# Kernel optimization log

Measured on AMD Instinct MI355X. Metric: run time of the kernel, lower is better.

## Reference

```python
import jax, jax.numpy as jnp
import numpy as np

B, L, D, U = 4, 1024, 64, 32

def setup_inputs() -> dict:
    key = jax.random.key(0)
    ks = jax.random.split(key, 6)
    inputs = jax.random.normal(ks[0], (B, L, D), dtype=jnp.float32)
    Wt = jax.random.normal(ks[1], (D, U), dtype=jnp.float32) * 0.1
    Wx = jax.random.normal(ks[2], (D, U), dtype=jnp.float32) * 0.1
    Wa = jax.random.normal(ks[3], (U, 1), dtype=jnp.float32) * 0.1
    bh = jax.random.normal(ks[4], (U,), dtype=jnp.float32) * 0.1
    ba = jax.random.normal(ks[5], (1,), dtype=jnp.float32) * 0.1
    return {"inputs": inputs, "Wt": Wt, "Wx": Wx, "Wa": Wa,
            "bh": bh, "ba": ba, "attention_width": 0}

def reference(inputs, Wt, Wx, Wa, bh, ba, attention_width):
    # Additive (Bahdanau) self-attention emission.
    q = inputs @ Wt                              # (B, L, U)
    k = inputs @ Wx                              # (B, L, U)
    # broadcast add -> (B, L, L, U), the dominant intermediate
    h = jnp.tanh(q[:, :, None, :] + k[:, None, :, :] + bh)
    e = jnp.squeeze(h @ Wa, axis=-1) + ba        # (B, L, L); ba broadcasts
    # NOTE: attention_width mask is dead code in the original forward -> ignored.
    # manual max-subtracted softmax with +1e-8 denominator (as in source)
    m = jnp.max(e, axis=-1, keepdims=True)
    ex = jnp.exp(e - m)
    a = ex / (jnp.sum(ex, axis=-1, keepdims=True) + 1e-8)
    v = jnp.einsum('bij,bjd->bid', a, inputs)    # (B, L, D)
    return v
```

## Files before the change

kernel.cpp:

```cpp
#include <hip/hip_runtime.h>

#define BB 4
#define LL 1024
#define DD 64
#define UU 32

__global__ __launch_bounds__(256) void precompute_kernel(
    const float* __restrict__ inp, const float* __restrict__ Wt,
    const float* __restrict__ Wx, const float* __restrict__ bh,
    float* __restrict__ Eq, float* __restrict__ Ek)
{
    __shared__ float s_in[8][DD];
    int t = threadIdx.x;
    int row0 = blockIdx.x * 8;
    if (t < 128) {
        ((float4*)s_in)[t] = ((const float4*)(inp + (size_t)row0 * DD))[t];
    }
    __syncthreads();
    int r = t >> 5;
    int u = t & 31;
    size_t row = row0 + r;
    float q = 0.f, k = 0.f;
#pragma unroll
    for (int d = 0; d < DD; ++d) {
        float x = s_in[r][d];
        q = fmaf(x, Wt[d * UU + u], q);
        k = fmaf(x, Wx[d * UU + u], k);
    }
    float eq = expf(2.f * (q + bh[u]));
    float ek = expf(2.f * k);
    Eq[row * UU + u] = eq;
    Ek[row * UU + u] = ek;
}

__device__ __forceinline__ float block_reduce_max(float v, float* sred, int t) {
#pragma unroll
    for (int m = 32; m >= 1; m >>= 1) v = fmaxf(v, __shfl_xor(v, m, 64));
    __syncthreads();
    if ((t & 63) == 0) sred[t >> 6] = v;
    __syncthreads();
    return fmaxf(fmaxf(sred[0], sred[1]), fmaxf(sred[2], sred[3]));
}
__device__ __forceinline__ float block_reduce_sum(float v, float* sred, int t) {
#pragma unroll
    for (int m = 32; m >= 1; m >>= 1) v += __shfl_xor(v, m, 64);
    __syncthreads();
    if ((t & 63) == 0) sred[t >> 6] = v;
    __syncthreads();
    return (sred[0] + sred[1]) + (sred[2] + sred[3]);
}

__global__ __launch_bounds__(256) void attn_kernel(
    const float* __restrict__ Eq, const float* __restrict__ Ek,
    const float* __restrict__ inp, const float* __restrict__ Wa,
    float* __restrict__ out)
{
    __shared__ float  s_a[LL][4];
    __shared__ float4 s_v[16][4][16];
    __shared__ float  s_red[4];

    int t  = threadIdx.x;
    int b  = blockIdx.x >> 8;
    int i0 = (blockIdx.x & 255) * 4;

    const float* ekb = Ek + (size_t)b * LL * UU;

    float e[4][4];
#pragma unroll
    for (int jj = 0; jj < 4; ++jj) {
        int j = jj * 256 + t;
        const float4* ekp = (const float4*)(ekb + (size_t)j * UU);
        float4 ekv[8];
#pragma unroll
        for (int u4 = 0; u4 < 8; ++u4) ekv[u4] = ekp[u4];
#pragma unroll
        for (int i = 0; i < 4; ++i) {
            const float* eqr = Eq + ((size_t)(b * LL + i0 + i)) * UU;
            float acc = 0.f;
#pragma unroll
            for (int u4 = 0; u4 < 8; ++u4) {
                const float* eqq = eqr + u4 * 4;
                const float* waq = Wa + u4 * 4;
                acc = fmaf(waq[0], __builtin_amdgcn_rcpf(fmaf(eqq[0], ekv[u4].x, 1.f)), acc);
                acc = fmaf(waq[1], __builtin_amdgcn_rcpf(fmaf(eqq[1], ekv[u4].y, 1.f)), acc);
                acc = fmaf(waq[2], __builtin_amdgcn_rcpf(fmaf(eqq[2], ekv[u4].z, 1.f)), acc);
                acc = fmaf(waq[3], __builtin_amdgcn_rcpf(fmaf(eqq[3], ekv[u4].w, 1.f)), acc);
            }
            e[i][jj] = -2.f * acc;
        }
    }

    float rs[4];
#pragma unroll
    for (int i = 0; i < 4; ++i) {
        float tm = fmaxf(fmaxf(e[i][0], e[i][1]), fmaxf(e[i][2], e[i][3]));
        float m = block_reduce_max(tm, s_red, t);
        float s = 0.f;
#pragma unroll
        for (int jj = 0; jj < 4; ++jj) {
            e[i][jj] = __expf(e[i][jj] - m);
            s += e[i][jj];
        }
        s = block_reduce_sum(s, s_red, t);
        rs[i] = 1.0f / (s + 1e-8f);
    }
#pragma unroll
    for (int jj = 0; jj < 4; ++jj) {
        float4 av;
        av.x = e[0][jj] * rs[0];
        av.y = e[1][jj] * rs[1];
        av.z = e[2][jj] * rs[2];
        av.w = e[3][jj] * rs[3];
        ((float4*)s_a)[jj * 256 + t] = av;
    }
    __syncthreads();

    int dq = t & 15;
    int g  = t >> 4;
    const float4* inp4 = (const float4*)(inp + (size_t)b * LL * DD);
    float4 v0 = {0,0,0,0}, v1 = {0,0,0,0}, v2 = {0,0,0,0}, v3 = {0,0,0,0};
#pragma unroll 4
    for (int jj = 0; jj < 64; ++jj) {
        int j = jj * 16 + g;
        float4 x  = inp4[j * 16 + dq];
        const float* ap = &s_a[j][0];
        float a0 = ap[0], a1 = ap[1], a2 = ap[2], a3 = ap[3];
        v0.x = fmaf(a0, x.x, v0.x); v0.y = fmaf(a0, x.y, v0.y);
        v0.z = fmaf(a0, x.z, v0.z); v0.w = fmaf(a0, x.w, v0.w);
        v1.x = fmaf(a1, x.x, v1.x); v1.y = fmaf(a1, x.y, v1.y);
        v1.z = fmaf(a1, x.z, v1.z); v1.w = fmaf(a1, x.w, v1.w);
        v2.x = fmaf(a2, x.x, v2.x); v2.y = fmaf(a2, x.y, v2.y);
        v2.z = fmaf(a2, x.z, v2.z); v2.w = fmaf(a2, x.w, v2.w);
        v3.x = fmaf(a3, x.x, v3.x); v3.y = fmaf(a3, x.y, v3.y);
        v3.z = fmaf(a3, x.z, v3.z); v3.w = fmaf(a3, x.w, v3.w);
    }
    s_v[g][0][dq] = v0;
    s_v[g][1][dq] = v1;
    s_v[g][2][dq] = v2;
    s_v[g][3][dq] = v3;
    __syncthreads();

    int i = t >> 6;
    int d = t & 63;
    const float* svf = (const float*)s_v;
    float r = 0.f;
#pragma unroll
    for (int g2 = 0; g2 < 16; ++g2) r += svf[g2 * 256 + i * 64 + d];
    out[((size_t)b * LL + (i0 + i)) * DD + d] = r;
}

extern "C" void kernel_launch(void* const* d_in, const int* in_sizes, int n_in,
                              void* d_out, int out_size, void* d_ws, size_t ws_size,
                              hipStream_t stream) {
    const float* inp = (const float*)d_in[0];
    const float* Wt  = (const float*)d_in[1];
    const float* Wx  = (const float*)d_in[2];
    const float* Wa  = (const float*)d_in[3];
    const float* bh  = (const float*)d_in[4];
    float* out = (float*)d_out;

    float* Eq = (float*)d_ws;
    float* Ek = Eq + (size_t)BB * LL * UU;

    precompute_kernel<<<BB * LL / 8, 256, 0, stream>>>(inp, Wt, Wx, bh, Eq, Ek);
    attn_kernel<<<BB * LL / 4, 256, 0, stream>>>(Eq, Ek, inp, Wa, out);
}
```

Baseline: 102.1 us.

## Combine four reciprocals into one, batch softmax reductions, stage weights in LDS

The attention score loop now merges four rcp(1+eq*ek) terms into one fraction, so a single reciprocal per four units replaces four. The Ek loads are reordered so each u4 chunk is prefetched across all four j columns. The per-row max and sum reductions are batched so each needs one pair of barriers instead of eight. The precompute kernel stages Wt and Wx in shared memory and uses fast exp. LDS for the probability and partial-output buffers is overlapped through a union, which adds an extra barrier. Multiplying four denominators together could overflow for large exponent values.

Measured after the change: 100.8 us. About the same (-1.2%).

```diff
diff --git a/kernel.cpp b/kernel.cpp
--- a/kernel.cpp
+++ b/kernel.cpp
@@ -4,6 +4,7 @@
 #define LL 1024
 #define DD 64
 #define UU 32
+#define TI 4
 
 __global__ __launch_bounds__(256) void precompute_kernel(
     const float* __restrict__ inp, const float* __restrict__ Wt,
@@ -11,10 +12,16 @@
     float* __restrict__ Eq, float* __restrict__ Ek)
 {
     __shared__ float s_in[8][DD];
+    __shared__ float s_wt[DD][UU];
+    __shared__ float s_wx[DD][UU];
     int t = threadIdx.x;
     int row0 = blockIdx.x * 8;
-    if (t < 128) {
+    if (t < 128)
         ((float4*)s_in)[t] = ((const float4*)(inp + (size_t)row0 * DD))[t];
+#pragma unroll
+    for (int p = 0; p < 2; ++p) {
+        ((float4*)s_wt)[p * 256 + t] = ((const float4*)Wt)[p * 256 + t];
+        ((float4*)s_wx)[p * 256 + t] = ((const float4*)Wx)[p * 256 + t];
     }
     __syncthreads();
     int r = t >> 5;
@@ -24,94 +31,138 @@
 #pragma unroll
     for (int d = 0; d < DD; ++d) {
         float x = s_in[r][d];
-        q = fmaf(x, Wt[d * UU + u], q);
-        k = fmaf(x, Wx[d * UU + u], k);
-    }
-    float eq = expf(2.f * (q + bh[u]));
-    float ek = expf(2.f * k);
-    Eq[row * UU + u] = eq;
-    Ek[row * UU + u] = ek;
+        q = fmaf(x, s_wt[d][u], q);
+        k = fmaf(x, s_wx[d][u], k);
+    }
+    Eq[row * UU + u] = __expf(2.f * (q + bh[u]));
+    Ek[row * UU + u] = __expf(2.f * k);
 }
 
-__device__ __forceinline__ float block_reduce_max(float v, float* sred, int t) {
-#pragma unroll
-    for (int m = 32; m >= 1; m >>= 1) v = fmaxf(v, __shfl_xor(v, m, 64));
-    __syncthreads();
-    if ((t & 63) == 0) sred[t >> 6] = v;
-    __syncthreads();
-    return fmaxf(fmaxf(sred[0], sred[1]), fmaxf(sred[2], sred[3]));
-}
-__device__ __forceinline__ float block_reduce_sum(float v, float* sred, int t) {
-#pragma unroll
-    for (int m = 32; m >= 1; m >>= 1) v += __shfl_xor(v, m, 64);
-    __syncthreads();
-    if ((t & 63) == 0) sred[t >> 6] = v;
-    __syncthreads();
-    return (sred[0] + sred[1]) + (sred[2] + sred[3]);
-}
+union ShMem {
+    float  a[LL][TI];
+    float4 v[16][TI][16];
+};
 
 __global__ __launch_bounds__(256) void attn_kernel(
     const float* __restrict__ Eq, const float* __restrict__ Ek,
     const float* __restrict__ inp, const float* __restrict__ Wa,
     float* __restrict__ out)
 {
-    __shared__ float  s_a[LL][4];
-    __shared__ float4 s_v[16][4][16];
-    __shared__ float  s_red[4];
+    __shared__ ShMem sh;
+    __shared__ float s_red[8][TI];
 
     int t  = threadIdx.x;
+    int w  = t >> 6;
     int b  = blockIdx.x >> 8;
-    int i0 = (blockIdx.x & 255) * 4;
-
-    const float* ekb = Ek + (size_t)b * LL * UU;
-
-    float e[4][4];
-#pragma unroll
-    for (int jj = 0; jj < 4; ++jj) {
-        int j = jj * 256 + t;
-        const float4* ekp = (const float4*)(ekb + (size_t)j * UU);
-        float4 ekv[8];
-#pragma unroll
-        for (int u4 = 0; u4 < 8; ++u4) ekv[u4] = ekp[u4];
-#pragma unroll
-        for (int i = 0; i < 4; ++i) {
-            const float* eqr = Eq + ((size_t)(b * LL + i0 + i)) * UU;
-            float acc = 0.f;
-#pragma unroll
-            for (int u4 = 0; u4 < 8; ++u4) {
-                const float* eqq = eqr + u4 * 4;
-                const float* waq = Wa + u4 * 4;
-                acc = fmaf(waq[0], __builtin_amdgcn_rcpf(fmaf(eqq[0], ekv[u4].x, 1.f)), acc);
-                acc = fmaf(waq[1], __builtin_amdgcn_rcpf(fmaf(eqq[1], ekv[u4].y, 1.f)), acc);
-                acc = fmaf(waq[2], __builtin_amdgcn_rcpf(fmaf(eqq[2], ekv[u4].z, 1.f)), acc);
-                acc = fmaf(waq[3], __builtin_amdgcn_rcpf(fmaf(eqq[3], ekv[u4].w, 1.f)), acc);
+    int i0 = (blockIdx.x & 255) * TI;
+
+    const float4* ekb4 = (const float4*)(Ek + (size_t)b * LL * UU);
+    const float*  eqb  = Eq + ((size_t)(b * LL + i0)) * UU;
+
+    float acc[TI][4];
+#pragma unroll
+    for (int i = 0; i < TI; ++i)
+#pragma unroll
+        for (int jj = 0; jj < 4; ++jj) acc[i][jj] = 0.f;
+
+    const float4* ekp[4];
+#pragma unroll
+    for (int jj = 0; jj < 4; ++jj) ekp[jj] = ekb4 + (size_t)(jj * 256 + t) * 8;
+
+    float4 cur[4], nxt[4];
+#pragma unroll
+    for (int jj = 0; jj < 4; ++jj) cur[jj] = ekp[jj][0];
+
+#pragma unroll
+    for (int u4 = 0; u4 < 8; ++u4) {
+        if (u4 < 7) {
+#pragma unroll
+            for (int jj = 0; jj < 4; ++jj) nxt[jj] = ekp[jj][u4 + 1];
+        }
+#pragma unroll
+        for (int i = 0; i < TI; ++i) {
+            const float* eqq = eqb + i * UU + u4 * 4;
+            float eq0 = eqq[0], eq1 = eqq[1], eq2 = eqq[2], eq3 = eqq[3];
+            const float* waq = Wa + u4 * 4;
+            float wa0 = waq[0], wa1 = waq[1], wa2 = waq[2], wa3 = waq[3];
+#pragma unroll
+            for (int jj = 0; jj < 4; ++jj) {
+                float4 ek = cur[jj];
+                float p  = fmaf(eq0, ek.x, 1.f);
+                float q  = fmaf(eq1, ek.y, 1.f);
+                float r  = fmaf(eq2, ek.z, 1.f);
+                float s  = fmaf(eq3, ek.w, 1.f);
+                float n01 = fmaf(wa0, q, wa1 * p);
+                float n23 = fmaf(wa2, s, wa3 * r);
+                float pq = p * q, rs = r * s;
+                float num = fmaf(n01, rs, n23 * pq);
+                float den = pq * rs;
+                acc[i][jj] = fmaf(num, __builtin_amdgcn_rcpf(den), acc[i][jj]);
             }
-            e[i][jj] = -2.f * acc;
-        }
-    }
-
-    float rs[4];
-#pragma unroll
-    for (int i = 0; i < 4; ++i) {
-        float tm = fmaxf(fmaxf(e[i][0], e[i][1]), fmaxf(e[i][2], e[i][3]));
-        float m = block_reduce_max(tm, s_red, t);
+        }
+        if (u4 < 7) {
+#pragma unroll
+            for (int jj = 0; jj < 4; ++jj) cur[jj] = nxt[jj];
+        }
+    }
+
+    float ev[TI][4];
+#pragma unroll
+    for (int i = 0; i < TI; ++i)
+#pragma unroll
+        for (int jj = 0; jj < 4; ++jj) ev[i][jj] = -2.f * acc[i][jj];
+
+    float wred[TI];
+#pragma unroll
+    for (int i = 0; i < TI; ++i) {
+        float v = fmaxf(fmaxf(ev[i][0], ev[i][1]), fmaxf(ev[i][2], ev[i][3]));
+#pragma unroll
+        for (int m = 32; m >= 1; m >>= 1) v = fmaxf(v, __shfl_xor(v, m, 64));
+        wred[i] = v;
+    }
+    if ((t & 63) == 0) {
+#pragma unroll
+        for (int i = 0; i < TI; ++i) s_red[w][i] = wred[i];
+    }
+    __syncthreads();
+    float m[TI];
+#pragma unroll
+    for (int i = 0; i < TI; ++i)
+        m[i] = fmaxf(fmaxf(s_red[0][i], s_red[1][i]),
+                     fmaxf(s_red[2][i], s_red[3][i]));
+
+#pragma unroll
+    for (int i = 0; i < TI; ++i) {
         float s = 0.f;
 #pragma unroll
         for (int jj = 0; jj < 4; ++jj) {
-            e[i][jj] = __expf(e[i][jj] - m);
-            s += e[i][jj];
-        }
-        s = block_reduce_sum(s, s_red, t);
+            ev[i][jj] = __expf(ev[i][jj] - m[i]);
+            s += ev[i][jj];
+        }
+#pragma unroll
+        for (int mm = 32; mm >= 1; mm >>= 1) s += __shfl_xor(s, mm, 64);
+        wred[i] = s;
+    }
+    if ((t & 63) == 0) {
+#pragma unroll
+        for (int i = 0; i < TI; ++i) s_red[4 + w][i] = wred[i];
+    }
+    __syncthreads();
+    float rs[TI];
+#pragma unroll
+    for (int i = 0; i < TI; ++i) {
+        float s = ((s_red[4][i] + s_red[5][i]) + (s_red[6][i] + s_red[7][i]));
         rs[i] = 1.0f / (s + 1e-8f);
     }
+
 #pragma unroll
     for (int jj = 0; jj < 4; ++jj) {
         float4 av;
-        av.x = e[0][jj] * rs[0];
-        av.y = e[1][jj] * rs[1];
-        av.z = e[2][jj] * rs[2];
-        av.w = e[3][jj] * rs[3];
-        ((float4*)s_a)[jj * 256 + t] = av;
+        av.x = ev[0][jj] * rs[0];
+        av.y = ev[1][jj] * rs[1];
+        av.z = ev[2][jj] * rs[2];
+        av.w = ev[3][jj] * rs[3];
+        ((float4*)sh.a)[jj * 256 + t] = av;
     }
     __syncthreads();
 
@@ -123,26 +174,26 @@
     for (int jj = 0; jj < 64; ++jj) {
         int j = jj * 16 + g;
         float4 x  = inp4[j * 16 + dq];
-        const float* ap = &s_a[j][0];
-        float a0 = ap[0], a1 = ap[1], a2 = ap[2], a3 = ap[3];
-        v0.x = fmaf(a0, x.x, v0.x); v0.y = fmaf(a0, x.y, v0.y);
-        v0.z = fmaf(a0, x.z, v0.z); v0.w = fmaf(a0, x.w, v0.w);
-        v1.x = fmaf(a1, x.x, v1.x); v1.y = fmaf(a1, x.y, v1.y);
-        v1.z = fmaf(a1, x.z, v1.z); v1.w = fmaf(a1, x.w, v1.w);
-        v2.x = fmaf(a2, x.x, v2.x); v2.y = fmaf(a2, x.y, v2.y);
-        v2.z = fmaf(a2, x.z, v2.z); v2.w = fmaf(a2, x.w, v2.w);
-        v3.x = fmaf(a3, x.x, v3.x); v3.y = fmaf(a3, x.y, v3.y);
-        v3.z = fmaf(a3, x.z, v3.z); v3.w = fmaf(a3, x.w, v3.w);
-    }
-    s_v[g][0][dq] = v0;
-    s_v[g][1][dq] = v1;
-    s_v[g][2][dq] = v2;
-    s_v[g][3][dq] = v3;
+        float4 av = ((const float4*)sh.a)[j];
+        v0.x = fmaf(av.x, x.x, v0.x); v0.y = fmaf(av.x, x.y, v0.y);
+        v0.z = fmaf(av.x, x.z, v0.z); v0.w = fmaf(av.x, x.w, v0.w);
+        v1.x = fmaf(av.y, x.x, v1.x); v1.y = fmaf(av.y, x.y, v1.y);
+        v1.z = fmaf(av.y, x.z, v1.z); v1.w = fmaf(av.y, x.w, v1.w);
+        v2.x = fmaf(av.z, x.x, v2.x); v2.y = fmaf(av.z, x.y, v2.y);
+        v2.z = fmaf(av.z, x.z, v2.z); v2.w = fmaf(av.z, x.w, v2.w);
+        v3.x = fmaf(av.w, x.x, v3.x); v3.y = fmaf(av.w, x.y, v3.y);
+        v3.z = fmaf(av.w, x.z, v3.z); v3.w = fmaf(av.w, x.w, v3.w);
+    }
+    __syncthreads();
+    sh.v[g][0][dq] = v0;
+    sh.v[g][1][dq] = v1;
+    sh.v[g][2][dq] = v2;
+    sh.v[g][3][dq] = v3;
     __syncthreads();
 
     int i = t >> 6;
     int d = t & 63;
-    const float* svf = (const float*)s_v;
+    const float* svf = (const float*)sh.v;
     float r = 0.f;
 #pragma unroll
     for (int g2 = 0; g2 < 16; ++g2) r += svf[g2 * 256 + i * 64 + d];
@@ -163,5 +214,5 @@
     float* Ek = Eq + (size_t)BB * LL * UU;
 
     precompute_kernel<<<BB * LL / 8, 256, 0, stream>>>(inp, Wt, Wx, bh, Eq, Ek);
-    attn_kernel<<<BB * LL / 4, 256, 0, stream>>>(Eq, Ek, inp, Wa, out);
+    attn_kernel<<<BB * LL / TI, 256, 0, stream>>>(Eq, Ek, inp, Wa, out);
 }
```
